# Optimization experiments

Measured on AMD Instinct MI355X. Metric: run time of the kernel, lower is better.

Reference implementation:

```python
import jax, jax.numpy as jnp
import numpy as np
from jax import lax

ENC_STRIDES = [8, 5, 4, 3]
ENC_CH = [1, 64, 128, 256, 512]
DEC_STRIDES = [3, 4, 5, 8]
DEC_CH = [512, 256, 128, 64, 1]
NUM_BOOKS = 8
BETA = 0.25


def _snake(x, alpha):
    # x: [B, C, T], alpha: [C]
    a = alpha[None, :, None]
    return x + (1.0 / a) * jnp.sin(a * x) ** 2


def _conv1d(x, w, b, stride, pad):
    # x: [B, Cin, T], w: [Cout, Cin, K] (torch layout)
    y = lax.conv_general_dilated(x, w, (stride,), [(pad, pad)],
                                 dimension_numbers=('NCH', 'OIH', 'NCH'))
    return y + b[None, :, None]


def _convT1d(x, w, b, stride, pad):
    # torch ConvTranspose1d weight [Cin, Cout, K] -> equivalent conv:
    # flip kernel, swap in/out, lhs_dilation=stride, padding k-1-p
    k = w.shape[-1]
    wc = jnp.flip(w, -1).transpose(1, 0, 2)  # [Cout, Cin, K]
    y = lax.conv_general_dilated(x, wc, (1,), [(k - 1 - pad, k - 1 - pad)],
                                 lhs_dilation=(stride,),
                                 dimension_numbers=('NCH', 'OIH', 'NCH'))
    return y + b[None, :, None]


def _rvq(z, pin_w, pin_b, pout_w, pout_b, cbs):
    # z: [B, 512, T]; cbs: [NUM_BOOKS, 1024, 128]
    residual = z
    codes = []
    total_loss = jnp.zeros((), z.dtype)
    for i in range(NUM_BOOKS):
        r = residual.transpose(0, 2, 1)            # [B, T, 512]
        zp = r @ pin_w.T + pin_b                   # [B, T, 128]
        cb = cbs[i]                                # [1024, 128]
        # squared euclidean distance (same argmin as torch.cdist)
        d2 = (jnp.sum(zp * zp, -1, keepdims=True)
              - 2.0 * jnp.einsum('btd,nd->btn', zp, cb)
              + jnp.sum(cb * cb, -1))
        idx = jnp.argmin(d2, -1)                   # [B, T]
        zq = cb[idx]                               # [B, T, 128]
        zq_st = zp + lax.stop_gradient(zq - zp)    # straight-through
        commit = jnp.mean((lax.stop_gradient(zq) - zp) ** 2)
        cbloss = jnp.mean((zq - lax.stop_gradient(zp)) ** 2)
        total_loss = total_loss + cbloss + BETA * commit
        zq_out = (zq_st @ pout_w.T + pout_b).transpose(0, 2, 1)  # [B, 512, T]
        residual = residual - zq_out
        codes.append(idx)
    return z - residual, jnp.stack(codes, 1), total_loss


def _forward(audio, ew, eb, ea, dw, db, da, pin_w, pin_b, pout_w, pout_b, cbs):
    x = audio
    for i, s in enumerate(ENC_STRIDES):
        x = _snake(_conv1d(x, ew[i], eb[i], s, s // 2), ea[i])
    z_q, codes, vq_loss = _rvq(x, pin_w, pin_b, pout_w, pout_b, cbs)
    x = z_q
    for i, s in enumerate(DEC_STRIDES):
        x = _convT1d(x, dw[i], db[i], s, s // 2)
        x = _snake(x, da[i]) if i < len(DEC_STRIDES) - 1 else jnp.tanh(x)
    return x, codes, vq_loss


def setup_inputs() -> dict:
    key = jax.random.key(0)
    ks = iter(jax.random.split(key, 64))
    inp = {}
    inp['audio'] = jax.random.normal(next(ks), (64, 1, 120000), jnp.float32)
    for i, s in enumerate(ENC_STRIDES):
        ci, co, k = ENC_CH[i], ENC_CH[i + 1], 2 * s
        sc = float(1.0 / np.sqrt(ci * k))
        inp[f'ew{i}'] = jax.random.uniform(next(ks), (co, ci, k), jnp.float32, -sc, sc)
        inp[f'eb{i}'] = jax.random.uniform(next(ks), (co,), jnp.float32, -sc, sc)
        inp[f'ea{i}'] = jnp.ones((co,), jnp.float32)
    for i, s in enumerate(DEC_STRIDES):
        ci, co, k = DEC_CH[i], DEC_CH[i + 1], 2 * s
        sc = float(1.0 / np.sqrt(ci * k))
        inp[f'dw{i}'] = jax.random.uniform(next(ks), (ci, co, k), jnp.float32, -sc, sc)
        inp[f'db{i}'] = jax.random.uniform(next(ks), (co,), jnp.float32, -sc, sc)
        if i < len(DEC_STRIDES) - 1:
            inp[f'da{i}'] = jnp.ones((co,), jnp.float32)
    sc_in = float(1.0 / np.sqrt(512))
    inp['pin_w'] = jax.random.uniform(next(ks), (128, 512), jnp.float32, -sc_in, sc_in)
    inp['pin_b'] = jax.random.uniform(next(ks), (128,), jnp.float32, -sc_in, sc_in)
    sc_out = float(1.0 / np.sqrt(128))
    inp['pout_w'] = jax.random.uniform(next(ks), (512, 128), jnp.float32, -sc_out, sc_out)
    inp['pout_b'] = jax.random.uniform(next(ks), (512,), jnp.float32, -sc_out, sc_out)
    inp['cbs'] = jax.random.uniform(next(ks), (NUM_BOOKS, 1024, 128), jnp.float32, -1.0 / 1024, 1.0 / 1024)
    return inp


def reference(audio, ew0, eb0, ea0, ew1, eb1, ea1, ew2, eb2, ea2, ew3, eb3, ea3,
              dw0, db0, da0, dw1, db1, da1, dw2, db2, da2, dw3, db3,
              pin_w, pin_b, pout_w, pout_b, cbs):
    return _forward(audio,
                    [ew0, ew1, ew2, ew3], [eb0, eb1, eb2, eb3], [ea0, ea1, ea2, ea3],
                    [dw0, dw1, dw2, dw3], [db0, db1, db2, db3], [da0, da1, da2],
                    pin_w, pin_b, pout_w, pout_b, cbs)
```

## Files before the change

kernel.cpp:

```cpp
#include <hip/hip_runtime.h>
#include <hip/hip_fp16.h>
#include <math.h>


#define T_RVQ 249
#define ROWS  (64*249)
#define NB    8
#define NCODE 1024

static inline int cdiv(int a, int b){ return (a+b-1)/b; }

__global__ void pack_w_conv(const float* __restrict__ w, float* __restrict__ wp,
                            int COUT, int CIN, int K){
  int i = blockIdx.x*256 + threadIdx.x;
  int tot = COUT*CIN*K;
  if (i >= tot) return;
  int co = i / (CIN*K); int r = i - co*(CIN*K);
  wp[(long)r*COUT + co] = w[i];
}
__global__ void pack_w_convT(const float* __restrict__ w, float* __restrict__ wp,
                             int CIN, int COUT, int K){
  int i = blockIdx.x*256 + threadIdx.x;
  int tot = CIN*COUT*K;
  if (i >= tot) return;
  int ci = i / (COUT*K); int r = i - ci*(COUT*K);
  int co = r / K; int j = r - co*K;
  wp[(long)(ci*K + j)*COUT + co] = w[i];
}
__global__ void prep_cn2f(const float* __restrict__ cbs, float* __restrict__ cn2){
  int i = blockIdx.x*256 + threadIdx.x;
  if (i >= NB*NCODE) return;
  const float* c = cbs + (long)i*128;
  float s = 0.f;
  for (int d=0; d<128; d++) s += c[d]*c[d];
  cn2[i] = s;
}
__global__ void zero_loss(double* p){ p[0] = 0.0; }

__global__ __launch_bounds__(256) void conv_e0e1(
    const float* __restrict__ audio,
    const float* __restrict__ w0,
    const float* __restrict__ b0v, const float* __restrict__ a0v,
    const float* __restrict__ wp1,
    const float* __restrict__ b1v, const float* __restrict__ a1v,
    double* __restrict__ out)
{
  constexpr int WIDTH = 63*5 + 10;
  constexpr int AW    = (WIDTH-1)*8 + 16;
  __shared__ double aud_s[AW];
  __shared__ double w0_s[64][16];
  __shared__ double b0_s[64], a0_s[64], i0_s[64];
  __shared__ double xs[4][WIDTH];
  __shared__ double ws[40][64];
  const int tid  = threadIdx.x;
  const int lo_t = tid & 15;
  const int co_t = tid >> 4;
  const int b    = blockIdx.z;
  const int co0  = blockIdx.y*64;
  const int lo0  = blockIdx.x*64;
  const int g0   = lo0*5 - 2;
  const long aud0 = (long)g0*8 - 4;
  for (int idx=tid; idx<AW; idx+=256){
    long s = aud0 + idx;
    aud_s[idx] = (s>=0 && s<120000) ? (double)audio[(long)b*120000 + s] : 0.0;
  }
  for (int idx=tid; idx<1024; idx+=256)
    w0_s[idx>>4][idx&15] = (double)w0[idx];
  if (tid < 64){
    b0_s[tid] = (double)b0v[tid];
    double a = (double)a0v[tid];
    a0_s[tid] = a; i0_s[tid] = 1.0/a;
  }
  double acc[4][4];
  #pragma unroll
  for (int c=0;c<4;c++){ acc[c][0]=0; acc[c][1]=0; acc[c][2]=0; acc[c][3]=0; }
  for (int ci0=0; ci0<64; ci0+=4){
    __syncthreads();
    for (int idx=tid; idx<4*WIDTH; idx+=256){
      int cich = idx / WIDTH, p = idx - cich*WIDTH;
      int ci = ci0 + cich;
      double v = b0_s[ci];
      #pragma unroll
      for (int j=0;j<16;j++) v += w0_s[ci][j]*aud_s[p*8 + j];
      double sn = sin(a0_s[ci]*v);
      double e0 = v + i0_s[ci]*sn*sn;
      int g = g0 + p;
      xs[cich][p] = (g>=0 && g<15000) ? e0 : 0.0;
    }
    for (int idx=tid; idx<40*64; idx+=256){
      int col = idx & 63, r = idx >> 6;
      ws[r][col] = (double)wp1[(long)(ci0*10 + r)*128 + co0 + col];
    }
    __syncthreads();
    for (int cich=0; cich<4; cich++){
      #pragma unroll
      for (int j=0;j<10;j++){
        double wv0 = ws[cich*10+j][co_t     ];
        double wv1 = ws[cich*10+j][co_t + 16];
        double wv2 = ws[cich*10+j][co_t + 32];
        double wv3 = ws[cich*10+j][co_t + 48];
        #pragma unroll
        for (int m=0;m<4;m++){
          double xv = xs[cich][(lo_t + 16*m)*5 + j];
          acc[0][m] += wv0*xv; acc[1][m] += wv1*xv;
          acc[2][m] += wv2*xv; acc[3][m] += wv3*xv;
        }
      }
    }
  }
  #pragma unroll
  for (int c=0;c<4;c++){
    int co = co0 + co_t + 16*c;
    double bv  = (double)b1v[co];
    double a   = (double)a1v[co];
    double inv = 1.0/a;
    #pragma unroll
    for (int m=0;m<4;m++){
      int lo = lo0 + lo_t + 16*m;
      if (lo < 2999){
        double v = acc[c][m] + bv;
        double sn = sin(a*v);
        v = v + inv*sn*sn;
        out[((long)b*128 + co)*2999 + lo] = v;
      }
    }
  }
}

template<int CIN,int COUT,int K,int S,int PAD,int CICH>
__global__ __launch_bounds__(256) void conv_enc(
    const double* __restrict__ x, const float* __restrict__ wp,
    const float* __restrict__ bias, const float* __restrict__ alpha,
    double* __restrict__ out, int Lin, int Lout)
{
  constexpr int WIDTH = 63*S + K;
  __shared__ double xs[CICH][WIDTH];
  __shared__ double ws[CICH*K][64];
  const int tid  = threadIdx.x;
  const int lo_t = tid & 15;
  const int co_t = tid >> 4;
  const int b    = blockIdx.z;
  const int co0  = blockIdx.y*64;
  const int lo0  = blockIdx.x*64;
  const int x0   = lo0*S - PAD;
  const long xb  = (long)b*CIN*Lin;
  double acc[4][4];
  #pragma unroll
  for (int c=0;c<4;c++){ acc[c][0]=0; acc[c][1]=0; acc[c][2]=0; acc[c][3]=0; }
  for (int ci0=0; ci0<CIN; ci0+=CICH){
    __syncthreads();
    for (int idx=tid; idx<CICH*WIDTH; idx+=256){
      int ci = idx / WIDTH, p = idx - ci*WIDTH;
      int g = x0 + p;
      xs[ci][p] = (g>=0 && g<Lin) ? x[xb + (long)(ci0+ci)*Lin + g] : 0.0;
    }
    for (int idx=tid; idx<CICH*K*64; idx+=256){
      int col = idx & 63, r = idx >> 6;
      ws[r][col] = (double)wp[(long)(ci0*K + r)*COUT + co0 + col];
    }
    __syncthreads();
    for (int ci=0; ci<CICH; ci++){
      #pragma unroll
      for (int j=0;j<K;j++){
        double w0 = ws[ci*K+j][co_t     ];
        double w1 = ws[ci*K+j][co_t + 16];
        double w2 = ws[ci*K+j][co_t + 32];
        double w3 = ws[ci*K+j][co_t + 48];
        #pragma unroll
        for (int m=0;m<4;m++){
          double xv = xs[ci][(lo_t + 16*m)*S + j];
          acc[0][m] += w0*xv; acc[1][m] += w1*xv;
          acc[2][m] += w2*xv; acc[3][m] += w3*xv;
        }
      }
    }
  }
  #pragma unroll
  for (int c=0;c<4;c++){
    int co = co0 + co_t + 16*c;
    double bv  = (double)bias[co];
    double a   = (double)alpha[co];
    double inv = 1.0/a;
    #pragma unroll
    for (int m=0;m<4;m++){
      int lo = lo0 + lo_t + 16*m;
      if (lo < Lout){
        double v = acc[c][m] + bv;
        double sn = sin(a*v);
        v = v + inv*sn*sn;
        out[((long)b*COUT + co)*Lout + lo] = v;
      }
    }
  }
}

template<int CIN,int COUT,int K,int S,int PAD,int CICH,
         int IMODE,int IS,int IT1,int IPAD,int T1OUT,int LOUT,typename OUTT>
__global__ __launch_bounds__(256) void convT_pm(
    const float* __restrict__ x, const float* __restrict__ wp,
    const float* __restrict__ bias, const float* __restrict__ alpha,
    OUTT* __restrict__ out, int Lin)
{
  __shared__ float xs[CICH][68];
  __shared__ float ws[CICH][2][64];
  const int tid  = threadIdx.x;
  const int lo_t = tid & 15;
  const int co_t = tid >> 4;
  const int bx   = blockIdx.x;
  const int r    = bx % S;
  const int t10  = (bx / S) * 64;
  const int b    = blockIdx.z;
  const int co0  = blockIdx.y*64;
  float acc[4][4];
  #pragma unroll
  for (int c=0;c<4;c++){ acc[c][0]=0; acc[c][1]=0; acc[c][2]=0; acc[c][3]=0; }
  for (int ci0=0; ci0<CIN; ci0+=CICH){
    __syncthreads();
    for (int idx=tid; idx<CICH*65; idx+=256){
      int ci = idx / 65, p = idx - ci*65;
      int t = t10 - 1 + p;
      float v = 0.f;
      if (t >= 0 && t < Lin){
        long bci = (long)b*CIN + ci0 + ci;
        if (IMODE == 0) v = x[bci*Lin + t];
        else { int u = t + IPAD; int rr = u % IS; int tt = u / IS;
               v = x[(bci*IS + rr)*IT1 + tt]; }
      }
      xs[ci][p] = v;
    }
    for (int idx=tid; idx<CICH*2*64; idx+=256){
      int col = idx & 63, q = idx >> 6;
      int ci = q >> 1, tap = q & 1;
      ws[ci][tap][col] = wp[(long)((ci0+ci)*K + r + tap*S)*COUT + co0 + col];
    }
    __syncthreads();
    for (int ci=0; ci<CICH; ci++){
      float4 wa = *(const float4*)&ws[ci][0][co_t*4];
      float4 wb = *(const float4*)&ws[ci][1][co_t*4];
      float4 xv = *(const float4*)&xs[ci][lo_t*4];
      float  xe = xs[ci][lo_t*4 + 4];
      float xp[5] = {xv.x, xv.y, xv.z, xv.w, xe};
      #pragma unroll
      for (int j=0;j<4;j++){
        float xa = xp[j+1];
        float xb2 = xp[j];
        acc[0][j] += wa.x*xa + wb.x*xb2;
        acc[1][j] += wa.y*xa + wb.y*xb2;
        acc[2][j] += wa.z*xa + wb.z*xb2;
        acc[3][j] += wa.w*xa + wb.w*xb2;
      }
    }
  }
  #pragma unroll
  for (int c=0;c<4;c++){
    int co = co0 + co_t*4 + c;
    float bv  = bias[co];
    float a   = alpha[co];
    float inv = 1.f/a;
    long obase = ((long)((long)b*COUT + co)*S + r)*T1OUT;
    #pragma unroll
    for (int j=0;j<4;j++){
      int t1 = t10 + lo_t*4 + j;
      int lo = t1*S + r - PAD;
      if (t1 < T1OUT && lo >= 0 && lo < LOUT){
        float v = acc[c][j] + bv;
        float sn = __sinf(a*v);
        v = v + inv*sn*sn;
        out[obase + t1] = OUTT(v);
      }
    }
  }
}

__global__ __launch_bounds__(256) void convT_last(
    const __half* __restrict__ x,
    const float* __restrict__ w,
    const float* __restrict__ bias,
    float* __restrict__ out)
{
  constexpr int LIN = 14961, LOUT = 119688, CIN = 64;
  __shared__ __align__(16) float xs[8][1028];
  __shared__ float ws[8][16];
  const int tid = threadIdx.x;
  const int b   = blockIdx.z;
  const int t10 = blockIdx.x*1024;
  float acc[4][8];
  #pragma unroll
  for (int u=0;u<4;u++) for (int rr=0;rr<8;rr++) acc[u][rr]=0.f;
  for (int ci0=0; ci0<CIN; ci0+=8){
    __syncthreads();
    for (int idx=tid; idx<8*1025; idx+=256){
      int ci = idx / 1025, p = idx - ci*1025;
      int t = t10 - 1 + p;
      float v = 0.f;
      if (t >= 0 && t < LIN){
        int u = t + 2; int rr = u % 5; int tt = u / 5;
        v = __half2float(x[((long)((long)b*CIN + ci0+ci)*5 + rr)*2993 + tt]);
      }
      xs[ci][p] = v;
    }
    if (tid < 128){
      int ci = tid >> 4, j = tid & 15;
      ws[ci][j] = w[(ci0+ci)*16 + j];
    }
    __syncthreads();
    #pragma unroll 2
    for (int ci=0; ci<8; ci++){
      float4 xv = *(const float4*)&xs[ci][tid*4];
      float  xe = xs[ci][tid*4 + 4];
      float xb_[5] = {xv.x, xv.y, xv.z, xv.w, xe};
      #pragma unroll
      for (int u=0;u<4;u++){
        float xprev = xb_[u];
        float xcur  = xb_[u+1];
        #pragma unroll
        for (int rr=0; rr<8; rr++)
          acc[u][rr] += ws[ci][rr]*xcur + ws[ci][rr+8]*xprev;
      }
    }
  }
  float bv = bias[0];
  #pragma unroll
  for (int u=0;u<4;u++){
    int t1 = t10 + tid*4 + u;
    #pragma unroll
    for (int rr=0;rr<8;rr++){
      int lo = t1*8 + rr - 4;
      if (lo >= 0 && lo < LOUT)
        out[(long)b*LOUT + lo] = tanhf(acc[u][rr] + bv);
    }
  }
}

__global__ void nv_transpose_f(const double* __restrict__ z, float* __restrict__ R){
  long i = (long)blockIdx.x*256 + threadIdx.x;
  if (i >= (long)ROWS*512) return;
  int row = (int)(i >> 9); int c = (int)(i & 511);
  int b = row / T_RVQ, t = row - b*T_RVQ;
  R[i] = (float)z[((long)b*512 + c)*T_RVQ + t];
}

__global__ __launch_bounds__(256) void rvq_proj_t(
    const float* __restrict__ R, const float* __restrict__ pin_w,
    const float* __restrict__ pin_b, float* __restrict__ zp)
{
  __shared__ float Rs[64][36];
  __shared__ float Ps[64][132];
  const int tid = threadIdx.x;
  const int row0 = blockIdx.x*32;
  const int d_t = tid & 31;
  const int r_t = tid >> 5;
  float acc[4][4];
  #pragma unroll
  for (int k=0;k<4;k++){ acc[k][0]=0; acc[k][1]=0; acc[k][2]=0; acc[k][3]=0; }
  for (int c0=0; c0<512; c0+=64){
    __syncthreads();
    for (int idx=tid; idx<2048; idx+=256){
      int c = idx & 63, r = idx >> 6;
      Rs[c][r] = R[(long)(row0+r)*512 + c0 + c];
    }
    for (int idx=tid; idx<8192; idx+=256){
      int c = idx & 63, d = idx >> 6;
      Ps[c][d] = pin_w[(long)d*512 + c0 + c];
    }
    __syncthreads();
    for (int c=0; c<64; c++){
      float4 rv = *(const float4*)&Rs[c][r_t*4];
      float4 wv = *(const float4*)&Ps[c][d_t*4];
      acc[0][0] += rv.x*wv.x; acc[0][1] += rv.x*wv.y; acc[0][2] += rv.x*wv.z; acc[0][3] += rv.x*wv.w;
      acc[1][0] += rv.y*wv.x; acc[1][1] += rv.y*wv.y; acc[1][2] += rv.y*wv.z; acc[1][3] += rv.y*wv.w;
      acc[2][0] += rv.z*wv.x; acc[2][1] += rv.z*wv.y; acc[2][2] += rv.z*wv.z; acc[2][3] += rv.z*wv.w;
      acc[3][0] += rv.w*wv.x; acc[3][1] += rv.w*wv.y; acc[3][2] += rv.w*wv.z; acc[3][3] += rv.w*wv.w;
    }
  }
  #pragma unroll
  for (int k=0;k<4;k++){
    int row = row0 + r_t*4 + k;
    #pragma unroll
    for (int j=0;j<4;j++){
      int d = d_t*4 + j;
      zp[(long)row*128 + d] = acc[k][j] + pin_b[d];
    }
  }
}

__global__ __launch_bounds__(256) void rvq_dist_t(
    const float* __restrict__ zp, const float* __restrict__ cb,
    const float* __restrict__ cn2, float* __restrict__ codes_out,
    int* __restrict__ codes_int, double* __restrict__ loss_acc, int book)
{
  __shared__ float zp_l[32][129];
  __shared__ float zp2_l[32];
  __shared__ float cb_s[32][132];
  __shared__ float cn2_s[128];
  __shared__ float sv[32][33];
  __shared__ int   si[32][33];
  __shared__ double ls[32];
  const int tid = threadIdx.x;
  const int row0 = blockIdx.x*32;
  const int n_t = tid & 31;
  const int r_t = tid >> 5;
  for (int idx=tid; idx<32*128; idx+=256){
    int r = idx >> 7, d = idx & 127;
    zp_l[r][d] = zp[(long)(row0+r)*128 + d];
  }
  __syncthreads();
  if (tid < 32){
    float s2 = 0.f;
    for (int d=0; d<128; d++) s2 += zp_l[tid][d]*zp_l[tid][d];
    zp2_l[tid] = s2;
  }
  float best[4]; int bi[4];
  #pragma unroll
  for (int k=0;k<4;k++){ best[k]=3.4e38f; bi[k]=0; }
  for (int tile=0; tile<8; tile++){
    __syncthreads();
    if (tid < 128) cn2_s[tid] = cn2[tile*128 + tid];
    float dot[4][4];
    #pragma unroll
    for (int k=0;k<4;k++){ dot[k][0]=0; dot[k][1]=0; dot[k][2]=0; dot[k][3]=0; }
    for (int dch=0; dch<4; dch++){
      __syncthreads();
      for (int idx=tid; idx<128*32; idx+=256){
        int dd = idx & 31, n = idx >> 5;
        cb_s[dd][n] = cb[(long)(tile*128 + n)*128 + dch*32 + dd];
      }
      __syncthreads();
      for (int dd=0; dd<32; dd++){
        float4 cv = *(const float4*)&cb_s[dd][n_t*4];
        float zr[4];
        #pragma unroll
        for (int k=0;k<4;k++) zr[k] = zp_l[r_t + 8*k][dch*32 + dd];
        #pragma unroll
        for (int k=0;k<4;k++){
          dot[k][0] += zr[k]*cv.x; dot[k][1] += zr[k]*cv.y;
          dot[k][2] += zr[k]*cv.z; dot[k][3] += zr[k]*cv.w;
        }
      }
    }
    #pragma unroll
    for (int k=0;k<4;k++){
      float z2 = zp2_l[r_t + 8*k];
      #pragma unroll
      for (int j=0;j<4;j++){
        int n = n_t*4 + j;
        float dist = (z2 - 2.0f*dot[k][j]) + cn2_s[n];
        int gn = tile*128 + n;
        if (dist < best[k]){ best[k]=dist; bi[k]=gn; }
      }
    }
  }
  __syncthreads();
  #pragma unroll
  for (int k=0;k<4;k++){
    sv[r_t + 8*k][n_t] = best[k];
    si[r_t + 8*k][n_t] = bi[k];
  }
  __syncthreads();
  if (tid < 32){
    float b2 = sv[tid][0]; int i2 = si[tid][0];
    for (int q=1; q<32; q++){
      float v = sv[tid][q]; int ii = si[tid][q];
      if (v < b2 || (v == b2 && ii < i2)){ b2=v; i2=ii; }
    }
    int row = row0 + tid;
    int bb = row / T_RVQ, t = row - bb*T_RVQ;
    codes_out[bb*(NB*T_RVQ) + book*T_RVQ + t] = (float)i2;
    codes_int[(long)row*NB + book] = i2;
    ls[tid] = (double)b2;
  }
  __syncthreads();
  if (tid == 0){
    double s = 0.0;
    for (int rr=0;rr<32;rr++) s += ls[rr];
    atomicAdd(loss_acc, s);
  }
}

__global__ __launch_bounds__(256) void rvq_update_t(
    float* __restrict__ R, const float* __restrict__ cb,
    const float* __restrict__ zp, const float* __restrict__ pout_w,
    const float* __restrict__ pout_b, const int* __restrict__ codes_int,
    int book)
{
  __shared__ float st_l[32][128];
  __shared__ float po_s[64][132];
  __shared__ int code_l[32];
  const int tid = threadIdx.x;
  const int row0 = blockIdx.x*32;
  if (tid < 32) code_l[tid] = codes_int[(long)(row0+tid)*NB + book];
  __syncthreads();
  for (int idx=tid; idx<32*128; idx+=256){
    int r = idx >> 7, d = idx & 127;
    float zpv = zp[(long)(row0+r)*128 + d];
    float zqv = cb[(long)code_l[r]*128 + d];
    st_l[r][d] = zpv + (zqv - zpv);
  }
  const int r_t = tid >> 3;
  const int cl  = tid & 7;
  for (int c0=0; c0<512; c0+=64){
    __syncthreads();
    for (int idx=tid; idx<64*128; idx+=256){
      int d = idx & 127, c = idx >> 7;
      po_s[c][d] = pout_w[(long)(c0+c)*128 + d];
    }
    __syncthreads();
    float s[8];
    #pragma unroll
    for (int ii=0;ii<8;ii++) s[ii] = 0.f;
    for (int d4=0; d4<128; d4+=4){
      float4 sv4 = *(const float4*)&st_l[r_t][d4];
      #pragma unroll
      for (int ii=0; ii<8; ii++){
        float4 wv4 = *(const float4*)&po_s[cl + 8*ii][d4];
        s[ii] += sv4.x*wv4.x; s[ii] += sv4.y*wv4.y;
        s[ii] += sv4.z*wv4.z; s[ii] += sv4.w*wv4.w;
      }
    }
    #pragma unroll
    for (int ii=0; ii<8; ii++){
      int c = c0 + cl + 8*ii;
      long gi = (long)(row0 + r_t)*512 + c;
      R[gi] = R[gi] - (s[ii] + pout_b[c]);
    }
  }
}

__global__ void make_zq(const double* __restrict__ z, const float* __restrict__ R,
                        float* __restrict__ zq){
  long i = (long)blockIdx.x*256 + threadIdx.x;
  if (i >= (long)ROWS*512) return;
  int row = (int)(i >> 9); int c = (int)(i & 511);
  int b = row / T_RVQ, t = row - b*T_RVQ;
  long zi = ((long)b*512 + c)*T_RVQ + t;
  zq[zi] = (float)z[zi] - R[i];
}

__global__ void loss_final(const double* __restrict__ loss_acc, float* __restrict__ out){
  out[0] = (float)(loss_acc[0] * (1.25 / 2039808.0));
}

extern "C" void kernel_launch(void* const* d_in, const int* in_sizes, int n_in,
                              void* d_out, int out_size, void* d_ws, size_t ws_size,
                              hipStream_t stream)
{
  (void)in_sizes; (void)n_in; (void)out_size; (void)ws_size;
  const float* audio  = (const float*)d_in[0];
  const float* ew0=(const float*)d_in[1],  *eb0=(const float*)d_in[2],  *ea0=(const float*)d_in[3];
  const float* ew1=(const float*)d_in[4],  *eb1=(const float*)d_in[5],  *ea1=(const float*)d_in[6];
  const float* ew2=(const float*)d_in[7],  *eb2=(const float*)d_in[8],  *ea2=(const float*)d_in[9];
  const float* ew3=(const float*)d_in[10], *eb3=(const float*)d_in[11], *ea3=(const float*)d_in[12];
  const float* dw0=(const float*)d_in[13], *db0=(const float*)d_in[14], *da0=(const float*)d_in[15];
  const float* dw1=(const float*)d_in[16], *db1=(const float*)d_in[17], *da1=(const float*)d_in[18];
  const float* dw2=(const float*)d_in[19], *db2=(const float*)d_in[20], *da2=(const float*)d_in[21];
  const float* dw3=(const float*)d_in[22], *db3=(const float*)d_in[23];
  const float* pin_w =(const float*)d_in[24], *pin_b =(const float*)d_in[25];
  const float* pout_w=(const float*)d_in[26], *pout_b=(const float*)d_in[27];
  const float* cbs   =(const float*)d_in[28];

  float* out_audio = (float*)d_out;
  float* out_codes = out_audio + 7660032;
  float* out_loss  = out_audio + 7787520;

  char* base = (char*)d_ws;
  double* z64    = (double*)(base);
  double* e1half = (double*)(base +  65273856);
  double* e2half = (double*)(base + 163545088);
  float*  R      = (float*) (base +  65273856);
  float*  zp_f   = (float*) (base +  97910784);
  float*  zq32   = (float*) (base + 106070400);
  float*  d0pm   = (float*) (base);
  float*  d1pm   = (float*) (base + 122683392);
  __half* d2pm   = (__half*)(base);
  char* p = base + 220856320;
  auto alloc = [&](size_t bytes)->char*{
    char* r = p; p += (bytes + 255) & ~(size_t)255; return r;
  };
  float* wpE1 = (float*)alloc((size_t)128*64*10*4);
  float* wpE2 = (float*)alloc((size_t)256*128*8*4);
  float* wpE3 = (float*)alloc((size_t)512*256*6*4);
  float* wpD0 = (float*)alloc((size_t)512*256*6*4);
  float* wpD1 = (float*)alloc((size_t)256*128*8*4);
  float* wpD2 = (float*)alloc((size_t)128*64*10*4);
  float* cn2f = (float*)alloc((size_t)NB*NCODE*4);
  int* codesI = (int*)  alloc((size_t)ROWS*NB*4);
  double* lossA=(double*)alloc(256);

  pack_w_conv <<<cdiv(128*64*10,256),256,0,stream>>>(ew1, wpE1, 128, 64, 10);
  pack_w_conv <<<cdiv(256*128*8,256),256,0,stream>>>(ew2, wpE2, 256, 128, 8);
  pack_w_conv <<<cdiv(512*256*6,256),256,0,stream>>>(ew3, wpE3, 512, 256, 6);
  pack_w_convT<<<cdiv(512*256*6,256),256,0,stream>>>(dw0, wpD0, 512, 256, 6);
  pack_w_convT<<<cdiv(256*128*8,256),256,0,stream>>>(dw1, wpD1, 256, 128, 8);
  pack_w_convT<<<cdiv(128*64*10,256),256,0,stream>>>(dw2, wpD2, 128, 64, 10);
  prep_cn2f  <<<cdiv(NB*NCODE,256),256,0,stream>>>(cbs, cn2f);
  zero_loss  <<<1,1,0,stream>>>(lossA);

  for (int h=0; h<2; h++){
    long b0 = 32L*h;
    conv_e0e1<<<dim3(cdiv(2999,64),2,32),256,0,stream>>>(
        audio + b0*120000, ew0, eb0, ea0, wpE1, eb1, ea1, e1half);
    conv_enc<128,256,8,4,2,8> <<<dim3(cdiv(749,64),4,32),256,0,stream>>>(
        e1half, wpE2, eb2, ea2, e2half, 2999, 749);
    conv_enc<256,512,6,3,1,8> <<<dim3(cdiv(249,64),8,32),256,0,stream>>>(
        e2half, wpE3, eb3, ea3, z64 + b0*512*249, 749, 249);
  }

  nv_transpose_f<<<cdiv(ROWS*512,256),256,0,stream>>>(z64, R);
  for (int bk=0; bk<NB; bk++){
    rvq_proj_t<<<ROWS/32,256,0,stream>>>(R, pin_w, pin_b, zp_f);
    rvq_dist_t<<<ROWS/32,256,0,stream>>>(zp_f, cbs + (long)bk*NCODE*128,
                                         cn2f + bk*NCODE, out_codes, codesI, lossA, bk);
    rvq_update_t<<<ROWS/32,256,0,stream>>>(R, cbs + (long)bk*NCODE*128, zp_f,
                                           pout_w, pout_b, codesI, bk);
  }
  make_zq<<<cdiv(ROWS*512,256),256,0,stream>>>(z64, R, zq32);

  convT_pm<512,256,6,3,1,16, 0,1,1,0, 250, 748, float>
      <<<dim3(cdiv(250,64)*3, 4, 64),256,0,stream>>>(zq32, wpD0, db0, da0, d0pm, 249);
  convT_pm<256,128,8,4,2,16, 1,3,250,1, 749, 2992, float>
      <<<dim3(cdiv(749,64)*4, 2, 64),256,0,stream>>>(d0pm, wpD1, db1, da1, d1pm, 748);
  convT_pm<128,64,10,5,2,16, 1,4,749,2, 2993, 14961, __half>
      <<<dim3(cdiv(2993,64)*5, 1, 64),256,0,stream>>>(d1pm, wpD2, db2, da2, d2pm, 2992);
  convT_last<<<dim3(cdiv(14962,1024),1,64),256,0,stream>>>(d2pm, dw3, db3, out_audio);

  loss_final<<<1,1,0,stream>>>(lossA, out_loss);
}
```

Baseline: 8.980 ms.

## Fuse transposed-conv phases per block to reuse input tile across phases

```diff
diff --git a/kernel.cpp b/kernel.cpp
--- a/kernel.cpp
+++ b/kernel.cpp
@@ -194,29 +194,30 @@
   }
 }
 
-template<int CIN,int COUT,int K,int S,int PAD,int CICH,
+template<int CIN,int COUT,int K,int S,int PAD,
          int IMODE,int IS,int IT1,int IPAD,int T1OUT,int LOUT,typename OUTT>
-__global__ __launch_bounds__(256) void convT_pm(
+__global__ __launch_bounds__(256) void convT_rm(
     const float* __restrict__ x, const float* __restrict__ wp,
     const float* __restrict__ bias, const float* __restrict__ alpha,
     OUTT* __restrict__ out, int Lin)
 {
-  __shared__ float xs[CICH][68];
-  __shared__ float ws[CICH][2][64];
+  __shared__ float xs[32][68];
+  __shared__ float ws[32][2][64];
   const int tid  = threadIdx.x;
   const int lo_t = tid & 15;
   const int co_t = tid >> 4;
-  const int bx   = blockIdx.x;
-  const int r    = bx % S;
-  const int t10  = (bx / S) * 64;
+  const int t10  = blockIdx.x*64;
   const int b    = blockIdx.z;
   const int co0  = blockIdx.y*64;
-  float acc[4][4];
-  #pragma unroll
-  for (int c=0;c<4;c++){ acc[c][0]=0; acc[c][1]=0; acc[c][2]=0; acc[c][3]=0; }
-  for (int ci0=0; ci0<CIN; ci0+=CICH){
-    __syncthreads();
-    for (int idx=tid; idx<CICH*65; idx+=256){
+  float acc[S][16];
+  #pragma unroll
+  for (int r=0;r<S;r++)
+    #pragma unroll
+    for (int q=0;q<16;q++) acc[r][q] = 0.f;
+
+  for (int ci0=0; ci0<CIN; ci0+=32){
+    __syncthreads();
+    for (int idx=tid; idx<32*65; idx+=256){
       int ci = idx / 65, p = idx - ci*65;
       int t = t10 - 1 + p;
       float v = 0.f;
@@ -228,45 +229,71 @@
       }
       xs[ci][p] = v;
     }
-    for (int idx=tid; idx<CICH*2*64; idx+=256){
-      int col = idx & 63, q = idx >> 6;
-      int ci = q >> 1, tap = q & 1;
-      ws[ci][tap][col] = wp[(long)((ci0+ci)*K + r + tap*S)*COUT + co0 + col];
-    }
-    __syncthreads();
-    for (int ci=0; ci<CICH; ci++){
-      float4 wa = *(const float4*)&ws[ci][0][co_t*4];
-      float4 wb = *(const float4*)&ws[ci][1][co_t*4];
-      float4 xv = *(const float4*)&xs[ci][lo_t*4];
-      float  xe = xs[ci][lo_t*4 + 4];
-      float xp[5] = {xv.x, xv.y, xv.z, xv.w, xe};
+    #pragma unroll
+    for (int r=0; r<S; r++){
+      __syncthreads();
+      for (int idx=tid; idx<32*2*64; idx+=256){
+        int col = idx & 63, q = idx >> 6;
+        int ci = q >> 1, tap = q & 1;
+        ws[ci][tap][col] = wp[(long)((ci0+ci)*K + r + tap*S)*COUT + co0 + col];
+      }
+      __syncthreads();
+      #pragma unroll 8
+      for (int ci=0; ci<32; ci++){
+        float4 wa = *(const float4*)&ws[ci][0][co_t*4];
+        float4 wb = *(const float4*)&ws[ci][1][co_t*4];
+        float4 xv = *(const float4*)&xs[ci][lo_t*4];
+        float  xe = xs[ci][lo_t*4 + 4];
+        float xp[5] = {xv.x, xv.y, xv.z, xv.w, xe};
+        #pragma unroll
+        for (int j=0;j<4;j++){
+          float xa = xp[j+1];
+          float xb2 = xp[j];
+          acc[r][0*4+j] += wa.x*xa + wb.x*xb2;
+          acc[r][1*4+j] += wa.y*xa + wb.y*xb2;
+          acc[r][2*4+j] += wa.z*xa + wb.z*xb2;
+          acc[r][3*4+j] += wa.w*xa + wb.w*xb2;
+        }
+      }
+    }
+  }
+
+  const int t1b = t10 + lo_t*4;
+  #pragma unroll
+  for (int r=0; r<S; r++){
+    #pragma unroll
+    for (int c=0; c<4; c++){
+      int co = co0 + co_t*4 + c;
+      float bv  = bias[co];
+      float a   = alpha[co];
+      float inv = 1.f/a;
+      long obase = ((long)((long)b*COUT + co)*S + r)*T1OUT;
+      float v4[4];
       #pragma unroll
       for (int j=0;j<4;j++){
-        float xa = xp[j+1];
-        float xb2 = xp[j];
-        acc[0][j] += wa.x*xa + wb.x*xb2;
-        acc[1][j] += wa.y*xa + wb.y*xb2;
-        acc[2][j] += wa.z*xa + wb.z*xb2;
-        acc[3][j] += wa.w*xa + wb.w*xb2;
-      }
-    }
-  }
-  #pragma unroll
-  for (int c=0;c<4;c++){
-    int co = co0 + co_t*4 + c;
-    float bv  = bias[co];
-    float a   = alpha[co];
-    float inv = 1.f/a;
-    long obase = ((long)((long)b*COUT + co)*S + r)*T1OUT;
-    #pragma unroll
-    for (int j=0;j<4;j++){
-      int t1 = t10 + lo_t*4 + j;
-      int lo = t1*S + r - PAD;
-      if (t1 < T1OUT && lo >= 0 && lo < LOUT){
-        float v = acc[c][j] + bv;
+        float v = acc[r][c*4+j] + bv;
         float sn = __sinf(a*v);
-        v = v + inv*sn*sn;
-        out[obase + t1] = OUTT(v);
+        v4[j] = v + inv*sn*sn;
+      }
+      int lo0v = t1b*S + r - PAD;
+      int lo3v = (t1b+3)*S + r - PAD;
+      if (t1b + 3 < T1OUT && lo0v >= 0 && lo3v < LOUT){
+        if constexpr (sizeof(OUTT) == 4){
+          *(float4*)&((float*)out)[obase + t1b] = make_float4(v4[0],v4[1],v4[2],v4[3]);
+        } else {
+          __half2 h01(__float2half(v4[0]), __float2half(v4[1]));
+          __half2 h23(__float2half(v4[2]), __float2half(v4[3]));
+          *(__half2*)&((__half*)out)[obase + t1b    ] = h01;
+          *(__half2*)&((__half*)out)[obase + t1b + 2] = h23;
+        }
+      } else {
+        #pragma unroll
+        for (int j=0;j<4;j++){
+          int t1 = t1b + j;
+          int lo = t1*S + r - PAD;
+          if (t1 < T1OUT && lo >= 0 && lo < LOUT)
+            out[obase + t1] = OUTT(v4[j]);
+        }
       }
     }
   }
@@ -615,12 +642,12 @@
   }
   make_zq<<<cdiv(ROWS*512,256),256,0,stream>>>(z64, R, zq32);
 
-  convT_pm<512,256,6,3,1,16, 0,1,1,0, 250, 748, float>
-      <<<dim3(cdiv(250,64)*3, 4, 64),256,0,stream>>>(zq32, wpD0, db0, da0, d0pm, 249);
-  convT_pm<256,128,8,4,2,16, 1,3,250,1, 749, 2992, float>
-      <<<dim3(cdiv(749,64)*4, 2, 64),256,0,stream>>>(d0pm, wpD1, db1, da1, d1pm, 748);
-  convT_pm<128,64,10,5,2,16, 1,4,749,2, 2993, 14961, __half>
-      <<<dim3(cdiv(2993,64)*5, 1, 64),256,0,stream>>>(d1pm, wpD2, db2, da2, d2pm, 2992);
+  convT_rm<512,256,6,3,1, 0,1,1,0, 250, 748, float>
+      <<<dim3(cdiv(250,64), 4, 64),256,0,stream>>>(zq32, wpD0, db0, da0, d0pm, 249);
+  convT_rm<256,128,8,4,2, 1,3,250,1, 749, 2992, float>
+      <<<dim3(cdiv(749,64), 2, 64),256,0,stream>>>(d0pm, wpD1, db1, da1, d1pm, 748);
+  convT_rm<128,64,10,5,2, 1,4,749,2, 2993, 14961, __half>
+      <<<dim3(cdiv(2993,64), 1, 64),256,0,stream>>>(d1pm, wpD2, db2, da2, d2pm, 2992);
   convT_last<<<dim3(cdiv(14962,1024),1,64),256,0,stream>>>(d2pm, dw3, db3, out_audio);
 
   loss_final<<<1,1,0,stream>>>(lossA, out_loss);
```

Result: faster. 8.329 ms (-7.2%).
